# Performance work log

Hardware: AMD Instinct MI355X
Metric: run time of the kernel (lower is better)

Reference implementation:

```python
import jax, jax.numpy as jnp
import numpy as np

B, D, H, K = 2048, 1024, 64, 3
SKIP = 4  # first 4 dims only accumulate into ai, produce no heads


def setup_inputs() -> dict:
    key = jax.random.key(0)
    ks = jax.random.split(key, 6)
    return {
        "x": jax.random.normal(ks[0], (B, D), jnp.float32),
        "W": jax.random.normal(ks[1], (H, D), jnp.float32) * (2.0 / (H + 1)) ** 0.5,
        "c": jax.random.normal(ks[2], (1, H), jnp.float32) * 0.0,
        "Vmean": jax.random.normal(ks[3], (D, H, K), jnp.float32) * (2.0 / (H + K)) ** 0.5,
        "Valpha": jax.random.normal(ks[4], (D, H, K), jnp.float32) * (2.0 / (H + K)) ** 0.5,
        "Vstd": jax.random.normal(ks[5], (D, H, K), jnp.float32) * (2.0 / (H + K)) ** 0.5,
        "bmean": jnp.zeros((D, K), jnp.float32),
        "balpha": jnp.zeros((D, K), jnp.float32),
        "bstd": jnp.zeros((D, K), jnp.float32),
    }


def reference(x, W, c, Vmean, Valpha, Vstd, bmean, balpha, bstd):
    # ai before processing dim d is c + sum_{j<d} x[:, j] * W[:, j]^T.
    # This is a cumulative sum of per-dim rank-1 contributions -> one cumsum.
    contrib = x[:, :, None] * W.T[None, :, :]          # [B, D, H]
    prefix = c[None, :, :] + jnp.cumsum(contrib, axis=1)  # prefix[:, d] = c + sum_{j<=d}
    # h_i for dim d (d >= SKIP) uses ai = prefix[:, d-1]
    h = jax.nn.relu(prefix[:, SKIP - 1:-1, :])          # [B, D-SKIP, H]

    mean = jnp.einsum("bdh,dhk->bdk", h, Vmean[SKIP:]) + bmean[SKIP:]
    std = jax.nn.sigmoid(
        jnp.einsum("bdh,dhk->bdk", h, Vstd[SKIP:]) + bstd[SKIP:]
    ) * 2.0 + 0.6  # 10**-1 + 0.5
    alpha = jax.nn.softmax(
        jnp.einsum("bdh,dhk->bdk", h, Valpha[SKIP:]) + balpha[SKIP:], axis=-1
    )
    return (mean, std, alpha)  # each [B, D-4, K]
```

## Files before the change

### kernel.cpp

```cpp
#include <hip/hip_runtime.h>
#include <hip/hip_bf16.h>

#define B 2048
#define D 1024
#define H 64
#define K 3
#define DOUT (D - 4)
#define T 64
#define DC 16

#if __has_builtin(__builtin_amdgcn_fdot2) && __has_builtin(__builtin_amdgcn_cvt_pkrtz)
#define HAS_DOT2 1
#else
#define HAS_DOT2 0
#endif
typedef __fp16 half2_t __attribute__((ext_vector_type(2)));

#define WS_S  0
#define WS_VP (T * B * H / 2)
#define WS_WT (WS_VP + D * 32 * 12)
#define WS_XT (WS_WT + D * H)

__device__ __forceinline__ unsigned short f2h_u(float f) {
    union { _Float16 h; unsigned short u; } v; v.h = (_Float16)f; return v.u;
}
__device__ __forceinline__ float h2f_u(unsigned short s) {
    union { unsigned short u; _Float16 h; } v; v.u = s; return (float)v.h;
}
__device__ __forceinline__ unsigned packh2(float lo, float hi) {
    union { _Float16 h[2]; unsigned u; } v;
    v.h[0] = (_Float16)lo; v.h[1] = (_Float16)hi; return v.u;
}
__device__ __forceinline__ half2_t as_h2(unsigned u) {
    union { unsigned u; half2_t h; } v; v.u = u; return v.h;
}

__global__ __launch_bounds__(256) void k_pack(const float* __restrict__ Vm,
                                              const float* __restrict__ Va,
                                              const float* __restrict__ Vs,
                                              unsigned* __restrict__ Vp) {
    int idx = blockIdx.x * 256 + threadIdx.x;
    const size_t hbase = ((size_t)(idx >> 5) * 64 + 2 * (idx & 31)) * 3;
    const float* pm = Vm + hbase;
    const float* ps = Vs + hbase;
    const float* pa = Va + hbase;
    unsigned o[12];
#pragma unroll
    for (int k = 0; k < 3; ++k) {
        o[k]     = packh2(pm[k], pm[3 + k]);
        o[3 + k] = packh2(ps[k], ps[3 + k]);
        o[6 + k] = packh2(pa[k], pa[3 + k]);
    }
    o[9] = 0u; o[10] = 0u; o[11] = 0u;
    uint4* dst = (uint4*)(Vp + (size_t)idx * 12);
    dst[0] = make_uint4(o[0], o[1], o[2], o[3]);
    dst[1] = make_uint4(o[4], o[5], o[6], o[7]);
    dst[2] = make_uint4(o[8], o[9], o[10], o[11]);
}

__global__ __launch_bounds__(256) void k_wt(const float* __restrict__ W,
                                            float* __restrict__ Wt) {
    __shared__ float tile[64][65];
    const int tx = threadIdx.x & 63;
    const int ty = threadIdx.x >> 6;
    const int d0 = blockIdx.x * 64;
#pragma unroll
    for (int r = 0; r < 64; r += 4)
        tile[r + ty][tx] = W[(size_t)(r + ty) * D + d0 + tx];
    __syncthreads();
#pragma unroll
    for (int r = 0; r < 64; r += 4)
        Wt[(size_t)(d0 + r + ty) * H + tx] = tile[tx][r + ty];
}

__global__ __launch_bounds__(256) void k_xt(const float* __restrict__ x,
                                            float* __restrict__ xT) {
    __shared__ float tile[64][65];
    const int tx = threadIdx.x & 63;
    const int ty = threadIdx.x >> 6;
    const int d0 = blockIdx.x * 64;
    const int b0 = blockIdx.y * 64;
#pragma unroll
    for (int r = 0; r < 64; r += 4)
        tile[r + ty][tx] = x[(size_t)(b0 + r + ty) * D + d0 + tx];
    __syncthreads();
#pragma unroll
    for (int r = 0; r < 64; r += 4)
        xT[(size_t)(d0 + r + ty) * B + b0 + tx] = tile[tx][r + ty];
}

__global__ __launch_bounds__(512) void k_prefix(const float* __restrict__ x,
                                                const float* __restrict__ W,
                                                const float* __restrict__ cvec,
                                                unsigned short* __restrict__ S) {
    __shared__ float wt[64 * 68];
    __shared__ float xl[8 * 64];
    const int tid  = threadIdx.x;
    const int lane = tid & 63;
    const int w    = tid >> 6;
    const int b    = blockIdx.x * 8 + w;

    float run = cvec[lane];
    for (int c = 0; c < 16; ++c) {
        __syncthreads();
        {
            const int h = tid >> 3, dc = (tid & 7) * 8;
            const float* src = W + (size_t)h * D + c * 64 + dc;
            float4 v0 = *(const float4*)src;
            float4 v1 = *(const float4*)(src + 4);
            float* dst = wt + h * 68 + dc;
            *(float4*)dst = v0;
            *(float4*)(dst + 4) = v1;
        }
        xl[w * 64 + lane] = x[(size_t)b * D + c * 64 + lane];
        __syncthreads();
#pragma unroll
        for (int dg = 0; dg < 16; ++dg) {
            if ((dg & 3) == 1) {
                const int t = 4 * c + (dg >> 2);
                S[((size_t)t * B + b) * H + lane] = f2h_u(run);
            }
            float4 w4 = *(const float4*)(wt + lane * 68 + dg * 4);
            float4 x4 = *(const float4*)(xl + w * 64 + dg * 4);
            run = fmaf(x4.x, w4.x, run);
            run = fmaf(x4.y, w4.y, run);
            run = fmaf(x4.z, w4.z, run);
            run = fmaf(x4.w, w4.w, run);
        }
    }
}

__global__ __launch_bounds__(256, 2) void k_main(const float* __restrict__ xT,
                                                 const unsigned short* __restrict__ S,
                                                 const unsigned* __restrict__ Vp,
                                                 const float* __restrict__ Wt,
                                                 const float* __restrict__ bm,
                                                 const float* __restrict__ ba,
                                                 const float* __restrict__ bs,
                                                 float* __restrict__ out) {
    __shared__ unsigned vsh[DC * 32 * 12];
    __shared__ float    wsh[DC * H];
    __shared__ float    bsh[DC * 9];

    const int tid    = threadIdx.x;
    const int lane   = tid & 63;
    const int w      = tid >> 6;
    const int t      = blockIdx.y;
    const int dstart = 16 * t + 4;
    const int b      = (blockIdx.x * 4 + w) * 64 + lane;
    const int dvalid = D - dstart;

    {
        const uint4* vsrc = (const uint4*)(Vp + (size_t)dstart * 384);
        uint4* vdst = (uint4*)vsh;
#pragma unroll
        for (int q = 0; q < 6; ++q) {
            const int j = q * 256 + tid;
            if (j * 4 < dvalid * 384) vdst[j] = vsrc[j];
        }
#pragma unroll
        for (int q = 0; q < 4; ++q) {
            const int idx = q * 256 + tid;
            if (idx < dvalid * 64) wsh[idx] = Wt[(size_t)dstart * 64 + idx];
        }
        if (tid < DC * 9) {
            const int dl = tid / 9, r = tid % 9;
            const int d = dstart + dl;
            if (d < D) {
                const float* p = (r < 3) ? (bm + (size_t)d * 3 + r)
                               : (r < 6) ? (bs + (size_t)d * 3 + (r - 3))
                                         : (ba + (size_t)d * 3 + (r - 6));
                bsh[tid] = *p;
            }
        }
    }

    float a[H];
    {
        const uint4* cp = (const uint4*)(S + ((size_t)t * B + b) * H);
#pragma unroll
        for (int q = 0; q < 8; ++q) {
            uint4 u = cp[q];
            a[q * 8 + 0] = h2f_u((unsigned short)(u.x & 0xffff));
            a[q * 8 + 1] = h2f_u((unsigned short)(u.x >> 16));
            a[q * 8 + 2] = h2f_u((unsigned short)(u.y & 0xffff));
            a[q * 8 + 3] = h2f_u((unsigned short)(u.y >> 16));
            a[q * 8 + 4] = h2f_u((unsigned short)(u.z & 0xffff));
            a[q * 8 + 5] = h2f_u((unsigned short)(u.z >> 16));
            a[q * 8 + 6] = h2f_u((unsigned short)(u.w & 0xffff));
            a[q * 8 + 7] = h2f_u((unsigned short)(u.w >> 16));
        }
    }
    __syncthreads();

    float* om = out + (size_t)b * DOUT * 3;
    float* os = om + (size_t)B * DOUT * 3;
    float* oa = os + (size_t)B * DOUT * 3;

    const int nq = (t == T - 1) ? 3 : 4;
    for (int q = 0; q < nq; ++q) {
        float bufm[12], bufs[12], bufa[12];
#pragma unroll
        for (int dl4 = 0; dl4 < 4; ++dl4) {
            const int dl = q * 4 + dl4;
            const float xv = xT[(size_t)(dstart + dl) * B + b];

            float acc[9];
#pragma unroll
            for (int k = 0; k < 9; ++k) acc[k] = 0.f;
            const unsigned* vb = vsh + dl * (32 * 12);
#pragma unroll
            for (int hp = 0; hp < 32; ++hp) {
#if HAS_DOT2
                half2_t h2 = __builtin_amdgcn_cvt_pkrtz(fmaxf(a[2 * hp], 0.f),
                                                        fmaxf(a[2 * hp + 1], 0.f));
                const uint4 u0 = *(const uint4*)(vb + hp * 12);
                const uint4 u1 = *(const uint4*)(vb + hp * 12 + 4);
                const unsigned u2 = vb[hp * 12 + 8];
                acc[0] = __builtin_amdgcn_fdot2(h2, as_h2(u0.x), acc[0], false);
                acc[1] = __builtin_amdgcn_fdot2(h2, as_h2(u0.y), acc[1], false);
                acc[2] = __builtin_amdgcn_fdot2(h2, as_h2(u0.z), acc[2], false);
                acc[3] = __builtin_amdgcn_fdot2(h2, as_h2(u0.w), acc[3], false);
                acc[4] = __builtin_amdgcn_fdot2(h2, as_h2(u1.x), acc[4], false);
                acc[5] = __builtin_amdgcn_fdot2(h2, as_h2(u1.y), acc[5], false);
                acc[6] = __builtin_amdgcn_fdot2(h2, as_h2(u1.z), acc[6], false);
                acc[7] = __builtin_amdgcn_fdot2(h2, as_h2(u1.w), acc[7], false);
                acc[8] = __builtin_amdgcn_fdot2(h2, as_h2(u2),   acc[8], false);
#else
                const float h0 = fmaxf(a[2 * hp], 0.f);
                const float h1 = fmaxf(a[2 * hp + 1], 0.f);
                const uint4 u0 = *(const uint4*)(vb + hp * 12);
                const uint4 u1 = *(const uint4*)(vb + hp * 12 + 4);
                const unsigned u2 = vb[hp * 12 + 8];
                unsigned uu[9] = {u0.x, u0.y, u0.z, u0.w, u1.x, u1.y, u1.z, u1.w, u2};
#pragma unroll
                for (int k = 0; k < 9; ++k) {
                    acc[k] = fmaf(h1, h2f_u((unsigned short)(uu[k] >> 16)),
                             fmaf(h0, h2f_u((unsigned short)(uu[k] & 0xffff)), acc[k]));
                }
#endif
            }
            bufm[dl4 * 3 + 0] = acc[0] + bsh[dl * 9 + 0];
            bufm[dl4 * 3 + 1] = acc[1] + bsh[dl * 9 + 1];
            bufm[dl4 * 3 + 2] = acc[2] + bsh[dl * 9 + 2];
#pragma unroll
            for (int k = 0; k < 3; ++k) {
                const float z = acc[3 + k] + bsh[dl * 9 + 3 + k];
                bufs[dl4 * 3 + k] = 2.f * __builtin_amdgcn_rcpf(1.f + __expf(-z)) + 0.6f;
            }
            {
                const float z0 = acc[6] + bsh[dl * 9 + 6];
                const float z1 = acc[7] + bsh[dl * 9 + 7];
                const float z2 = acc[8] + bsh[dl * 9 + 8];
                const float mx = fmaxf(z0, fmaxf(z1, z2));
                const float e0 = __expf(z0 - mx);
                const float e1 = __expf(z1 - mx);
                const float e2 = __expf(z2 - mx);
                const float inv = __builtin_amdgcn_rcpf(e0 + e1 + e2);
                bufa[dl4 * 3 + 0] = e0 * inv;
                bufa[dl4 * 3 + 1] = e1 * inv;
                bufa[dl4 * 3 + 2] = e2 * inv;
            }
            const float* wp = wsh + dl * H;
#pragma unroll
            for (int h = 0; h < H; h += 4) {
                float4 wv = *(const float4*)(wp + h);
                a[h]     = fmaf(xv, wv.x, a[h]);
                a[h + 1] = fmaf(xv, wv.y, a[h + 1]);
                a[h + 2] = fmaf(xv, wv.z, a[h + 2]);
                a[h + 3] = fmaf(xv, wv.w, a[h + 3]);
            }
        }
        const size_t off = (size_t)(16 * t + 4 * q) * 3;
#pragma unroll
        for (int qd = 0; qd < 3; ++qd) {
            *(float4*)(om + off + qd * 4) = make_float4(bufm[qd*4], bufm[qd*4+1], bufm[qd*4+2], bufm[qd*4+3]);
            *(float4*)(os + off + qd * 4) = make_float4(bufs[qd*4], bufs[qd*4+1], bufs[qd*4+2], bufs[qd*4+3]);
            *(float4*)(oa + off + qd * 4) = make_float4(bufa[qd*4], bufa[qd*4+1], bufa[qd*4+2], bufa[qd*4+3]);
        }
    }
}

extern "C" void kernel_launch(void* const* d_in, const int* in_sizes, int n_in,
                              void* d_out, int out_size, void* d_ws, size_t ws_size,
                              hipStream_t stream) {
    const float* x  = (const float*)d_in[0];
    const float* W  = (const float*)d_in[1];
    const float* c  = (const float*)d_in[2];
    const float* Vm = (const float*)d_in[3];
    const float* Va = (const float*)d_in[4];
    const float* Vs = (const float*)d_in[5];
    const float* bm = (const float*)d_in[6];
    const float* ba = (const float*)d_in[7];
    const float* bs = (const float*)d_in[8];
    float* out = (float*)d_out;

    float* wsf = (float*)d_ws;
    unsigned short* S = (unsigned short*)(wsf + WS_S);
    unsigned* Vp = (unsigned*)(wsf + WS_VP);
    float* Wt = wsf + WS_WT;
    float* xT = wsf + WS_XT;

    k_pack<<<dim3(D * 32 / 256), dim3(256), 0, stream>>>(Vm, Va, Vs, Vp);
    k_wt<<<dim3(D / 64), dim3(256), 0, stream>>>(W, Wt);
    k_xt<<<dim3(D / 64, B / 64), dim3(256), 0, stream>>>(x, xT);
    k_prefix<<<dim3(B / 8), dim3(512), 0, stream>>>(x, W, c, S);
    k_main<<<dim3(B / 256, T), dim3(256), 0, stream>>>(xT, S, Vp, Wt, bm, ba, bs, out);
}
```

Measured before the change: 181.0 us.

## Compute head projections with bf16 MFMA and drop transpose kernels

Replaces the per-thread fp16 dot2 projection of the 64 hidden units onto 9 outputs with MFMA 16x16x32 bf16 instructions. V is repacked into MFMA operand layout and the bias is folded into the accumulator init. The activation state is redistributed across lanes to match the MFMA fragment layout. x and W are now loaded directly into shared memory per block, so the separate transpose kernels go away and fewer kernels launch. In exchange, V and the activations drop to bf16 precision, and most lanes sit idle in the epilogue because only 9 of the 16 output rows matter.

```diff
diff --git a/kernel.cpp b/kernel.cpp
--- a/kernel.cpp
+++ b/kernel.cpp
@@ -4,22 +4,15 @@
 #define B 2048
 #define D 1024
 #define H 64
-#define K 3
 #define DOUT (D - 4)
 #define T 64
 #define DC 16
 
-#if __has_builtin(__builtin_amdgcn_fdot2) && __has_builtin(__builtin_amdgcn_cvt_pkrtz)
-#define HAS_DOT2 1
-#else
-#define HAS_DOT2 0
-#endif
-typedef __fp16 half2_t __attribute__((ext_vector_type(2)));
+typedef __attribute__((ext_vector_type(8))) short short8;
+typedef __attribute__((ext_vector_type(4))) float f32x4;
 
 #define WS_S  0
-#define WS_VP (T * B * H / 2)
-#define WS_WT (WS_VP + D * 32 * 12)
-#define WS_XT (WS_WT + D * H)
+#define WS_VB (T * B * H / 2)
 
 __device__ __forceinline__ unsigned short f2h_u(float f) {
     union { _Float16 h; unsigned short u; } v; v.h = (_Float16)f; return v.u;
@@ -27,66 +20,46 @@
 __device__ __forceinline__ float h2f_u(unsigned short s) {
     union { unsigned short u; _Float16 h; } v; v.u = s; return (float)v.h;
 }
-__device__ __forceinline__ unsigned packh2(float lo, float hi) {
-    union { _Float16 h[2]; unsigned u; } v;
-    v.h[0] = (_Float16)lo; v.h[1] = (_Float16)hi; return v.u;
-}
-__device__ __forceinline__ half2_t as_h2(unsigned u) {
-    union { unsigned u; half2_t h; } v; v.u = u; return v.h;
-}
+__device__ __forceinline__ unsigned short f2bf(float f) {
+    union { float f; unsigned int u; } v; v.f = f;
+    unsigned int r = (v.u + 0x7FFFu + ((v.u >> 16) & 1u)) >> 16;
+    return (unsigned short)r;
+}
+__device__ __forceinline__ unsigned cvtpk_bf16(float lo, float hi) {
+    unsigned d;
+    asm("v_cvt_pk_bf16_f32 %0, %1, %2" : "=v"(d) : "v"(lo), "v"(hi));
+    return d;
+}
+
+union U8 { unsigned u[4]; short8 s; };
 
 __global__ __launch_bounds__(256) void k_pack(const float* __restrict__ Vm,
                                               const float* __restrict__ Va,
                                               const float* __restrict__ Vs,
-                                              unsigned* __restrict__ Vp) {
-    int idx = blockIdx.x * 256 + threadIdx.x;
-    const size_t hbase = ((size_t)(idx >> 5) * 64 + 2 * (idx & 31)) * 3;
-    const float* pm = Vm + hbase;
-    const float* ps = Vs + hbase;
-    const float* pa = Va + hbase;
-    unsigned o[12];
-#pragma unroll
-    for (int k = 0; k < 3; ++k) {
-        o[k]     = packh2(pm[k], pm[3 + k]);
-        o[3 + k] = packh2(ps[k], ps[3 + k]);
-        o[6 + k] = packh2(pa[k], pa[3 + k]);
-    }
-    o[9] = 0u; o[10] = 0u; o[11] = 0u;
-    uint4* dst = (uint4*)(Vp + (size_t)idx * 12);
-    dst[0] = make_uint4(o[0], o[1], o[2], o[3]);
-    dst[1] = make_uint4(o[4], o[5], o[6], o[7]);
-    dst[2] = make_uint4(o[8], o[9], o[10], o[11]);
-}
-
-__global__ __launch_bounds__(256) void k_wt(const float* __restrict__ W,
-                                            float* __restrict__ Wt) {
-    __shared__ float tile[64][65];
-    const int tx = threadIdx.x & 63;
-    const int ty = threadIdx.x >> 6;
-    const int d0 = blockIdx.x * 64;
-#pragma unroll
-    for (int r = 0; r < 64; r += 4)
-        tile[r + ty][tx] = W[(size_t)(r + ty) * D + d0 + tx];
-    __syncthreads();
-#pragma unroll
-    for (int r = 0; r < 64; r += 4)
-        Wt[(size_t)(d0 + r + ty) * H + tx] = tile[tx][r + ty];
-}
-
-__global__ __launch_bounds__(256) void k_xt(const float* __restrict__ x,
-                                            float* __restrict__ xT) {
-    __shared__ float tile[64][65];
-    const int tx = threadIdx.x & 63;
-    const int ty = threadIdx.x >> 6;
-    const int d0 = blockIdx.x * 64;
-    const int b0 = blockIdx.y * 64;
-#pragma unroll
-    for (int r = 0; r < 64; r += 4)
-        tile[r + ty][tx] = x[(size_t)(b0 + r + ty) * D + d0 + tx];
-    __syncthreads();
-#pragma unroll
-    for (int r = 0; r < 64; r += 4)
-        xT[(size_t)(d0 + r + ty) * B + b0 + tx] = tile[tx][r + ty];
+                                              uint4* __restrict__ VbP) {
+    const int idx = blockIdx.x * 256 + threadIdx.x;
+    const int l   = idx & 63;
+    const int ks  = (idx >> 6) & 1;
+    const int d   = idx >> 7;
+    const int m   = l & 15;
+    const int h0  = ks * 32 + (l >> 4) * 8;
+
+    const float* src = nullptr;
+    int k = 0;
+    if (m < 3)                { src = Vm; k = m; }
+    else if (m >= 4 && m < 7) { src = Vs; k = m - 4; }
+    else if (m >= 8 && m < 11){ src = Va; k = m - 8; }
+
+    unsigned u[4] = {0u, 0u, 0u, 0u};
+    if (src) {
+#pragma unroll
+        for (int i = 0; i < 4; ++i) {
+            unsigned short lo = f2bf(src[((size_t)d * H + h0 + 2 * i) * 3 + k]);
+            unsigned short hi = f2bf(src[((size_t)d * H + h0 + 2 * i + 1) * 3 + k]);
+            u[i] = ((unsigned)hi << 16) | lo;
+        }
+    }
+    VbP[idx] = make_uint4(u[0], u[1], u[2], u[3]);
 }
 
 __global__ __launch_bounds__(512) void k_prefix(const float* __restrict__ x,
@@ -130,153 +103,178 @@
     }
 }
 
-__global__ __launch_bounds__(256, 2) void k_main(const float* __restrict__ xT,
+__global__ __launch_bounds__(256, 2) void k_main(const float* __restrict__ x,
+                                                 const float* __restrict__ W,
                                                  const unsigned short* __restrict__ S,
-                                                 const unsigned* __restrict__ Vp,
-                                                 const float* __restrict__ Wt,
+                                                 const uint4* __restrict__ VbP,
                                                  const float* __restrict__ bm,
                                                  const float* __restrict__ ba,
                                                  const float* __restrict__ bs,
                                                  float* __restrict__ out) {
-    __shared__ unsigned vsh[DC * 32 * 12];
-    __shared__ float    wsh[DC * H];
-    __shared__ float    bsh[DC * 9];
+    __shared__ short8 vbsh[DC][2][64];
+    __shared__ float  wshf[DC][64];
+    __shared__ float  xsf[DC][256];
+    __shared__ float  bshf[DC][16];
 
     const int tid    = threadIdx.x;
     const int lane   = tid & 63;
     const int w      = tid >> 6;
     const int t      = blockIdx.y;
+    const int bx     = blockIdx.x;
     const int dstart = 16 * t + 4;
-    const int b      = (blockIdx.x * 4 + w) * 64 + lane;
     const int dvalid = D - dstart;
+    const int r      = lane & 15;
+    const int qq     = lane >> 4;
 
     {
-        const uint4* vsrc = (const uint4*)(Vp + (size_t)dstart * 384);
-        uint4* vdst = (uint4*)vsh;
-#pragma unroll
-        for (int q = 0; q < 6; ++q) {
+        const uint4* vsrc = VbP + (size_t)dstart * 128;
+        uint4* vdst = (uint4*)vbsh;
+#pragma unroll
+        for (int q = 0; q < 8; ++q) {
             const int j = q * 256 + tid;
-            if (j * 4 < dvalid * 384) vdst[j] = vsrc[j];
-        }
-#pragma unroll
-        for (int q = 0; q < 4; ++q) {
-            const int idx = q * 256 + tid;
-            if (idx < dvalid * 64) wsh[idx] = Wt[(size_t)dstart * 64 + idx];
-        }
-        if (tid < DC * 9) {
-            const int dl = tid / 9, r = tid % 9;
+            if (j < dvalid * 128) vdst[j] = vsrc[j];
+        }
+        {
+            const int h = tid >> 2, part = tid & 3;
+            if (dstart + part * 4 < D) {
+                float4 v = *(const float4*)(W + (size_t)h * D + dstart + part * 4);
+                wshf[part * 4 + 0][h] = v.x;
+                wshf[part * 4 + 1][h] = v.y;
+                wshf[part * 4 + 2][h] = v.z;
+                wshf[part * 4 + 3][h] = v.w;
+            }
+        }
+        {
+            const float* xr = x + (size_t)(bx * 256 + tid) * D + dstart;
+#pragma unroll
+            for (int part = 0; part < 4; ++part) {
+                if (dstart + part * 4 < D) {
+                    float4 v = *(const float4*)(xr + part * 4);
+                    xsf[part * 4 + 0][tid] = v.x;
+                    xsf[part * 4 + 1][tid] = v.y;
+                    xsf[part * 4 + 2][tid] = v.z;
+                    xsf[part * 4 + 3][tid] = v.w;
+                }
+            }
+        }
+        {
+            const int dl = tid >> 4, m = tid & 15;
             const int d = dstart + dl;
+            float v = 0.f;
             if (d < D) {
-                const float* p = (r < 3) ? (bm + (size_t)d * 3 + r)
-                               : (r < 6) ? (bs + (size_t)d * 3 + (r - 3))
-                                         : (ba + (size_t)d * 3 + (r - 6));
-                bsh[tid] = *p;
-            }
-        }
-    }
-
-    float a[H];
-    {
-        const uint4* cp = (const uint4*)(S + ((size_t)t * B + b) * H);
-#pragma unroll
-        for (int q = 0; q < 8; ++q) {
-            uint4 u = cp[q];
-            a[q * 8 + 0] = h2f_u((unsigned short)(u.x & 0xffff));
-            a[q * 8 + 1] = h2f_u((unsigned short)(u.x >> 16));
-            a[q * 8 + 2] = h2f_u((unsigned short)(u.y & 0xffff));
-            a[q * 8 + 3] = h2f_u((unsigned short)(u.y >> 16));
-            a[q * 8 + 4] = h2f_u((unsigned short)(u.z & 0xffff));
-            a[q * 8 + 5] = h2f_u((unsigned short)(u.z >> 16));
-            a[q * 8 + 6] = h2f_u((unsigned short)(u.w & 0xffff));
-            a[q * 8 + 7] = h2f_u((unsigned short)(u.w >> 16));
+                if (m < 3)                 v = bm[(size_t)d * 3 + m];
+                else if (m >= 4 && m < 7)  v = bs[(size_t)d * 3 + m - 4];
+                else if (m >= 8 && m < 11) v = ba[(size_t)d * 3 + m - 8];
+            }
+            bshf[dl][m] = v;
+        }
+    }
+
+    float a_[4][2][8];
+#pragma unroll
+    for (int bt = 0; bt < 4; ++bt) {
+#pragma unroll
+        for (int ks = 0; ks < 2; ++ks) {
+            const unsigned short* sp =
+                S + ((size_t)t * B + bx * 256 + w * 64 + bt * 16 + r) * H + ks * 32 + qq * 8;
+            uint4 u = *(const uint4*)sp;
+            a_[bt][ks][0] = h2f_u((unsigned short)(u.x & 0xffff));
+            a_[bt][ks][1] = h2f_u((unsigned short)(u.x >> 16));
+            a_[bt][ks][2] = h2f_u((unsigned short)(u.y & 0xffff));
+            a_[bt][ks][3] = h2f_u((unsigned short)(u.y >> 16));
+            a_[bt][ks][4] = h2f_u((unsigned short)(u.z & 0xffff));
+            a_[bt][ks][5] = h2f_u((unsigned short)(u.z >> 16));
+            a_[bt][ks][6] = h2f_u((unsigned short)(u.w & 0xffff));
+            a_[bt][ks][7] = h2f_u((unsigned short)(u.w >> 16));
         }
     }
     __syncthreads();
 
-    float* om = out + (size_t)b * DOUT * 3;
-    float* os = om + (size_t)B * DOUT * 3;
-    float* oa = os + (size_t)B * DOUT * 3;
-
     const int nq = (t == T - 1) ? 3 : 4;
-    for (int q = 0; q < nq; ++q) {
-        float bufm[12], bufs[12], bufa[12];
-#pragma unroll
-        for (int dl4 = 0; dl4 < 4; ++dl4) {
-            const int dl = q * 4 + dl4;
-            const float xv = xT[(size_t)(dstart + dl) * B + b];
-
-            float acc[9];
-#pragma unroll
-            for (int k = 0; k < 9; ++k) acc[k] = 0.f;
-            const unsigned* vb = vsh + dl * (32 * 12);
-#pragma unroll
-            for (int hp = 0; hp < 32; ++hp) {
-#if HAS_DOT2
-                half2_t h2 = __builtin_amdgcn_cvt_pkrtz(fmaxf(a[2 * hp], 0.f),
-                                                        fmaxf(a[2 * hp + 1], 0.f));
-                const uint4 u0 = *(const uint4*)(vb + hp * 12);
-                const uint4 u1 = *(const uint4*)(vb + hp * 12 + 4);
-                const unsigned u2 = vb[hp * 12 + 8];
-                acc[0] = __builtin_amdgcn_fdot2(h2, as_h2(u0.x), acc[0], false);
-                acc[1] = __builtin_amdgcn_fdot2(h2, as_h2(u0.y), acc[1], false);
-                acc[2] = __builtin_amdgcn_fdot2(h2, as_h2(u0.z), acc[2], false);
-                acc[3] = __builtin_amdgcn_fdot2(h2, as_h2(u0.w), acc[3], false);
-                acc[4] = __builtin_amdgcn_fdot2(h2, as_h2(u1.x), acc[4], false);
-                acc[5] = __builtin_amdgcn_fdot2(h2, as_h2(u1.y), acc[5], false);
-                acc[6] = __builtin_amdgcn_fdot2(h2, as_h2(u1.z), acc[6], false);
-                acc[7] = __builtin_amdgcn_fdot2(h2, as_h2(u1.w), acc[7], false);
-                acc[8] = __builtin_amdgcn_fdot2(h2, as_h2(u2),   acc[8], false);
-#else
-                const float h0 = fmaxf(a[2 * hp], 0.f);
-                const float h1 = fmaxf(a[2 * hp + 1], 0.f);
-                const uint4 u0 = *(const uint4*)(vb + hp * 12);
-                const uint4 u1 = *(const uint4*)(vb + hp * 12 + 4);
-                const unsigned u2 = vb[hp * 12 + 8];
-                unsigned uu[9] = {u0.x, u0.y, u0.z, u0.w, u1.x, u1.y, u1.z, u1.w, u2};
-#pragma unroll
-                for (int k = 0; k < 9; ++k) {
-                    acc[k] = fmaf(h1, h2f_u((unsigned short)(uu[k] >> 16)),
-                             fmaf(h0, h2f_u((unsigned short)(uu[k] & 0xffff)), acc[k]));
+    for (int qd = 0; qd < nq; ++qd) {
+        float buf[4][12];
+#pragma unroll
+        for (int d4 = 0; d4 < 4; ++d4) {
+            const int dl = qd * 4 + d4;
+
+            U8 bf[4][2];
+#pragma unroll
+            for (int bt = 0; bt < 4; ++bt)
+#pragma unroll
+                for (int ks = 0; ks < 2; ++ks)
+#pragma unroll
+                    for (int i = 0; i < 4; ++i)
+                        bf[bt][ks].u[i] = cvtpk_bf16(fmaxf(a_[bt][ks][2 * i], 0.f),
+                                                     fmaxf(a_[bt][ks][2 * i + 1], 0.f));
+
+            short8 A0 = vbsh[dl][0][lane];
+            short8 A1 = vbsh[dl][1][lane];
+            f32x4 bias4 = ((const f32x4*)&bshf[dl][0])[qq];
+
+            f32x4 acc[4];
+#pragma unroll
+            for (int bt = 0; bt < 4; ++bt) {
+                acc[bt] = __builtin_amdgcn_mfma_f32_16x16x32_bf16(A0, bf[bt][0].s, bias4, 0, 0, 0);
+                acc[bt] = __builtin_amdgcn_mfma_f32_16x16x32_bf16(A1, bf[bt][1].s, acc[bt], 0, 0, 0);
+            }
+
+#pragma unroll
+            for (int bt = 0; bt < 4; ++bt) {
+                float z0 = acc[bt][0], z1 = acc[bt][1], z2 = acc[bt][2];
+                float o0 = z0, o1 = z1, o2 = z2;
+                if (qq == 1) {
+                    o0 = 2.f * __builtin_amdgcn_rcpf(1.f + __expf(-z0)) + 0.6f;
+                    o1 = 2.f * __builtin_amdgcn_rcpf(1.f + __expf(-z1)) + 0.6f;
+                    o2 = 2.f * __builtin_amdgcn_rcpf(1.f + __expf(-z2)) + 0.6f;
+                } else if (qq == 2) {
+                    float mx = fmaxf(z0, fmaxf(z1, z2));
+                    float e0 = __expf(z0 - mx);
+                    float e1 = __expf(z1 - mx);
+                    float e2 = __expf(z2 - mx);
+                    float inv = __builtin_amdgcn_rcpf(e0 + e1 + e2);
+                    o0 = e0 * inv; o1 = e1 * inv; o2 = e2 * inv;
                 }
-#endif
-            }
-            bufm[dl4 * 3 + 0] = acc[0] + bsh[dl * 9 + 0];
-            bufm[dl4 * 3 + 1] = acc[1] + bsh[dl * 9 + 1];
-            bufm[dl4 * 3 + 2] = acc[2] + bsh[dl * 9 + 2];
-#pragma unroll
-            for (int k = 0; k < 3; ++k) {
-                const float z = acc[3 + k] + bsh[dl * 9 + 3 + k];
-                bufs[dl4 * 3 + k] = 2.f * __builtin_amdgcn_rcpf(1.f + __expf(-z)) + 0.6f;
-            }
-            {
-                const float z0 = acc[6] + bsh[dl * 9 + 6];
-                const float z1 = acc[7] + bsh[dl * 9 + 7];
-                const float z2 = acc[8] + bsh[dl * 9 + 8];
-                const float mx = fmaxf(z0, fmaxf(z1, z2));
-                const float e0 = __expf(z0 - mx);
-                const float e1 = __expf(z1 - mx);
-                const float e2 = __expf(z2 - mx);
-                const float inv = __builtin_amdgcn_rcpf(e0 + e1 + e2);
-                bufa[dl4 * 3 + 0] = e0 * inv;
-                bufa[dl4 * 3 + 1] = e1 * inv;
-                bufa[dl4 * 3 + 2] = e2 * inv;
-            }
-            const float* wp = wsh + dl * H;
-#pragma unroll
-            for (int h = 0; h < H; h += 4) {
-                float4 wv = *(const float4*)(wp + h);
-                a[h]     = fmaf(xv, wv.x, a[h]);
-                a[h + 1] = fmaf(xv, wv.y, a[h + 1]);
-                a[h + 2] = fmaf(xv, wv.z, a[h + 2]);
-                a[h + 3] = fmaf(xv, wv.w, a[h + 3]);
-            }
-        }
-        const size_t off = (size_t)(16 * t + 4 * q) * 3;
-#pragma unroll
-        for (int qd = 0; qd < 3; ++qd) {
-            *(float4*)(om + off + qd * 4) = make_float4(bufm[qd*4], bufm[qd*4+1], bufm[qd*4+2], bufm[qd*4+3]);
-            *(float4*)(os + off + qd * 4) = make_float4(bufs[qd*4], bufs[qd*4+1], bufs[qd*4+2], bufs[qd*4+3]);
-            *(float4*)(oa + off + qd * 4) = make_float4(bufa[qd*4], bufa[qd*4+1], bufa[qd*4+2], bufa[qd*4+3]);
+                buf[bt][d4 * 3 + 0] = o0;
+                buf[bt][d4 * 3 + 1] = o1;
+                buf[bt][d4 * 3 + 2] = o2;
+            }
+
+            float4 w0a = *(const float4*)&wshf[dl][qq * 8];
+            float4 w0b = *(const float4*)&wshf[dl][qq * 8 + 4];
+            float4 w1a = *(const float4*)&wshf[dl][32 + qq * 8];
+            float4 w1b = *(const float4*)&wshf[dl][32 + qq * 8 + 4];
+#pragma unroll
+            for (int bt = 0; bt < 4; ++bt) {
+                const float xv = xsf[dl][w * 64 + bt * 16 + r];
+                a_[bt][0][0] = fmaf(xv, w0a.x, a_[bt][0][0]);
+                a_[bt][0][1] = fmaf(xv, w0a.y, a_[bt][0][1]);
+                a_[bt][0][2] = fmaf(xv, w0a.z, a_[bt][0][2]);
+                a_[bt][0][3] = fmaf(xv, w0a.w, a_[bt][0][3]);
+                a_[bt][0][4] = fmaf(xv, w0b.x, a_[bt][0][4]);
+                a_[bt][0][5] = fmaf(xv, w0b.y, a_[bt][0][5]);
+                a_[bt][0][6] = fmaf(xv, w0b.z, a_[bt][0][6]);
+                a_[bt][0][7] = fmaf(xv, w0b.w, a_[bt][0][7]);
+                a_[bt][1][0] = fmaf(xv, w1a.x, a_[bt][1][0]);
+                a_[bt][1][1] = fmaf(xv, w1a.y, a_[bt][1][1]);
+                a_[bt][1][2] = fmaf(xv, w1a.z, a_[bt][1][2]);
+                a_[bt][1][3] = fmaf(xv, w1a.w, a_[bt][1][3]);
+                a_[bt][1][4] = fmaf(xv, w1b.x, a_[bt][1][4]);
+                a_[bt][1][5] = fmaf(xv, w1b.y, a_[bt][1][5]);
+                a_[bt][1][6] = fmaf(xv, w1b.z, a_[bt][1][6]);
+                a_[bt][1][7] = fmaf(xv, w1b.w, a_[bt][1][7]);
+            }
+        }
+
+        if (qq < 3) {
+            float* ob = out + (size_t)qq * ((size_t)B * DOUT * 3);
+            const size_t ioff = (size_t)(16 * t + 4 * qd) * 3;
+#pragma unroll
+            for (int bt = 0; bt < 4; ++bt) {
+                float* p = ob + (size_t)(bx * 256 + w * 64 + bt * 16 + r) * (DOUT * 3) + ioff;
+                *(float4*)(p + 0) = make_float4(buf[bt][0], buf[bt][1], buf[bt][2], buf[bt][3]);
+                *(float4*)(p + 4) = make_float4(buf[bt][4], buf[bt][5], buf[bt][6], buf[bt][7]);
+                *(float4*)(p + 8) = make_float4(buf[bt][8], buf[bt][9], buf[bt][10], buf[bt][11]);
+            }
         }
     }
 }
@@ -297,13 +295,9 @@
 
     float* wsf = (float*)d_ws;
     unsigned short* S = (unsigned short*)(wsf + WS_S);
-    unsigned* Vp = (unsigned*)(wsf + WS_VP);
-    float* Wt = wsf + WS_WT;
-    float* xT = wsf + WS_XT;
-
-    k_pack<<<dim3(D * 32 / 256), dim3(256), 0, stream>>>(Vm, Va, Vs, Vp);
-    k_wt<<<dim3(D / 64), dim3(256), 0, stream>>>(W, Wt);
-    k_xt<<<dim3(D / 64, B / 64), dim3(256), 0, stream>>>(x, xT);
+    uint4* VbP = (uint4*)(wsf + WS_VB);
+
+    k_pack<<<dim3(D * 2 * 64 / 256), dim3(256), 0, stream>>>(Vm, Va, Vs, VbP);
     k_prefix<<<dim3(B / 8), dim3(512), 0, stream>>>(x, W, c, S);
-    k_main<<<dim3(B / 256, T), dim3(256), 0, stream>>>(xT, S, Vp, Wt, bm, ba, bs, out);
-}
+    k_main<<<dim3(B / 256, T), dim3(256), 0, stream>>>(x, W, S, VbP, bm, ba, bs, out);
+}
```

Result: faster. 163.3 us (-9.7%).
